# Optimization experiments

Hardware: AMD Instinct MI355X
Metric: run time of the kernel (lower is better)

## Reference

```python
import jax, jax.numpy as jnp
import numpy as np

D_K = 64

def setup_inputs() -> dict:
    key = jax.random.key(0)
    kq, kk, kv, km = jax.random.split(key, 4)
    B, H, S, D = 2, 16, 2048, D_K
    Q = jax.random.normal(kq, (B, H, S, D), dtype=jnp.float32)
    K = jax.random.normal(kk, (B, H, S, D), dtype=jnp.float32)
    V = jax.random.normal(kv, (B, H, S, D), dtype=jnp.float32)
    attn_mask = jax.random.bernoulli(km, 0.9, (B, H, S))  # True = valid
    return {"Q": Q, "K": K, "V": V, "attn_mask": attn_mask}

def reference(Q, K, V, attn_mask):
    # scores: [B, H, S, S]
    scores = jnp.einsum('bhqd,bhkd->bhqk', Q, K) / np.sqrt(D_K).astype(np.float32)
    fill = jnp.float32(1e-9)
    # mask rows (query positions) then columns (key positions), as in original
    scores = jnp.where(attn_mask[..., :, None], scores, fill)
    scores = jnp.where(attn_mask[..., None, :], scores, fill)
    attn = jax.nn.softmax(scores, axis=-1)
    context = jnp.einsum('bhqk,bhkd->bhqd', attn, V)
    return (context, attn)
```

## Files before the change

### kernel.cpp

```cpp
#include <hip/hip_runtime.h>

#define B_DIM 2
#define H_DIM 16
#define S_DIM 2048
#define D_DIM 64

constexpr int QB = 128;
constexpr int KB = 64;
constexpr int NT = S_DIM / KB;
constexpr float CL2E = 0.18033688011112042f;

typedef __attribute__((ext_vector_type(8))) short short8;
typedef __attribute__((ext_vector_type(4))) float f32x4;
typedef __attribute__((ext_vector_type(2))) unsigned uint2v;

__device__ __forceinline__ unsigned pkbf(float lo, float hi) {
  unsigned r;
  asm("v_cvt_pk_bf16_f32 %0, %1, %2" : "=v"(r) : "v"(lo), "v"(hi));
  return r;
}

__device__ __forceinline__ float fexp2(float x) {
  float r;
  asm("v_exp_f32 %0, %1" : "=v"(r) : "v"(x));
  return r;
}

__device__ __forceinline__ void barrier_lds() {
  asm volatile("s_waitcnt lgkmcnt(0)" ::: "memory");
  __builtin_amdgcn_s_barrier();
  asm volatile("" ::: "memory");
}

__global__ __launch_bounds__(256, 2)
void sdpa_kernel(const float* __restrict__ Qp, const float* __restrict__ Kp,
                 const float* __restrict__ Vp, const int* __restrict__ maskp,
                 float* __restrict__ ctx, float* __restrict__ attn)
{
  __shared__ __align__(16) unsigned short sK[2][KB * 64];
  __shared__ __align__(16) unsigned short sV[2][64 * KB];
  __shared__ __align__(16) unsigned short sP[2][4][32 * 64];

  const int tid  = threadIdx.x;
  const int wave = tid >> 6;
  const int lane = tid & 63;
  const int c = lane & 15;
  const int g = lane >> 4;

  const int bid = (blockIdx.x & 7) * 64 + (blockIdx.x >> 3);
  const int bh = bid >> 4;
  const int qt = bid & 15;
  const int q0 = qt * QB + wave * 32;
  const size_t bhS = (size_t)bh * S_DIM;

  const int key = tid >> 2;
  const int dq  = (tid & 3) << 4;
  const int kp  = (tid & 31) << 1;
  const int dq8 = (tid >> 5) << 3;

  short8 qf[2][2];
  #pragma unroll
  for (int m = 0; m < 2; ++m)
    #pragma unroll
    for (int kk = 0; kk < 2; ++kk) {
      const float* src = Qp + (bhS + (size_t)(q0 + m*16 + c)) * D_DIM + kk*32 + g*8;
      float4 a = ((const float4*)src)[0];
      float4 b = ((const float4*)src)[1];
      union { unsigned u[4]; short8 s; } w;
      w.u[0] = pkbf(a.x, a.y); w.u[1] = pkbf(a.z, a.w);
      w.u[2] = pkbf(b.x, b.y); w.u[3] = pkbf(b.z, b.w);
      qf[m][kk] = w.s;
    }

  float rvS[2];
  #pragma unroll
  for (int m = 0; m < 2; ++m)
    rvS[m] = maskp[bhS + q0 + m*16 + c] ? CL2E : 0.0f;

  float4 kr0, kr1, kr2, kr3;
  float4 vA0, vA1, vB0, vB1;
  unsigned kmr;

  auto load_k = [&](int kt_) {
    const float* s = Kp + (bhS + (size_t)(kt_ * KB + key)) * D_DIM + dq;
    kr0 = ((const float4*)s)[0]; kr1 = ((const float4*)s)[1];
    kr2 = ((const float4*)s)[2]; kr3 = ((const float4*)s)[3];
    kmr = maskp[bhS + kt_ * KB + key] ? 0xFFFFFFFFu : 0u;
  };
  auto load_v = [&](int kt_) {
    const float* s0 = Vp + (bhS + (size_t)(kt_ * KB + kp)) * D_DIM + dq8;
    vA0 = ((const float4*)s0)[0]; vA1 = ((const float4*)s0)[1];
    vB0 = ((const float4*)(s0 + D_DIM))[0]; vB1 = ((const float4*)(s0 + D_DIM))[1];
  };
  auto write_k = [&](int buf) {
    union { unsigned u[4]; short8 s; } w0, w1;
    w0.u[0] = pkbf(kr0.x, kr0.y) & kmr; w0.u[1] = pkbf(kr0.z, kr0.w) & kmr;
    w0.u[2] = pkbf(kr1.x, kr1.y) & kmr; w0.u[3] = pkbf(kr1.z, kr1.w) & kmr;
    w1.u[0] = pkbf(kr2.x, kr2.y) & kmr; w1.u[1] = pkbf(kr2.z, kr2.w) & kmr;
    w1.u[2] = pkbf(kr3.x, kr3.y) & kmr; w1.u[3] = pkbf(kr3.z, kr3.w) & kmr;
    const int sw = (key & 7) << 3;
    *(short8*)&sK[buf][key * 64 + (dq ^ sw)]       = w0.s;
    *(short8*)&sK[buf][key * 64 + ((dq + 8) ^ sw)] = w1.s;
  };
  auto write_v = [&](int buf) {
    float fa[8], fb[8];
    *(float4*)&fa[0] = vA0; *(float4*)&fa[4] = vA1;
    *(float4*)&fb[0] = vB0; *(float4*)&fb[4] = vB1;
    #pragma unroll
    for (int e = 0; e < 8; ++e) {
      const int d = dq8 + e;
      *(unsigned*)&sV[buf][d * KB + (kp ^ ((d & 7) << 3))] = pkbf(fa[e], fb[e]);
    }
  };

  float lsum[2] = {0.0f, 0.0f};

  load_k(0);
  for (int kt = 0; kt < NT; ++kt) {
    const int cur = kt & 1;
    write_k(cur);
    if (kt + 1 < NT) load_k(kt + 1);
    barrier_lds();

    short8 kf[4][2];
    #pragma unroll
    for (int n = 0; n < 4; ++n) {
      const int k2 = n*16 + c;
      const int sw = (c & 7) << 3;
      #pragma unroll
      for (int kk = 0; kk < 2; ++kk)
        kf[n][kk] = *(const short8*)&sK[cur][k2*64 + ((kk*32 + g*8) ^ sw)];
    }

    f32x4 sacc[4][2];
    #pragma unroll
    for (int n = 0; n < 4; ++n)
      #pragma unroll
      for (int m = 0; m < 2; ++m) sacc[n][m] = 0.0f;
    __builtin_amdgcn_s_setprio(1);
    #pragma unroll
    for (int n = 0; n < 4; ++n)
      #pragma unroll
      for (int m = 0; m < 2; ++m)
        #pragma unroll
        for (int kk = 0; kk < 2; ++kk)
          sacc[n][m] = __builtin_amdgcn_mfma_f32_16x16x32_bf16(kf[n][kk], qf[m][kk], sacc[n][m], 0, 0, 0);
    __builtin_amdgcn_s_setprio(0);

    #pragma unroll
    for (int m = 0; m < 2; ++m)
      #pragma unroll
      for (int n = 0; n < 4; ++n)
        #pragma unroll
        for (int e = 0; e < 4; ++e)
          lsum[m] += fexp2(sacc[n][m][e] * rvS[m]);
  }

  float Lm[2];
  #pragma unroll
  for (int m = 0; m < 2; ++m) {
    float v = lsum[m];
    v += __shfl_xor(v, 16);
    v += __shfl_xor(v, 32);
    Lm[m] = -__log2f(v);
  }

  f32x4 oacc[2][4];
  #pragma unroll
  for (int m = 0; m < 2; ++m)
    #pragma unroll
    for (int n = 0; n < 4; ++n) oacc[m][n] = 0.0f;

  const int rh  = lane >> 4;
  const int c16 = lane & 15;
  float* const abase = attn + (bhS + (size_t)q0) * S_DIM;

  auto copyout = [&](int pb, int kt_) {
    const unsigned short* const Pp = sP[pb][wave];
    float* const at = abase + kt_*KB;
    #pragma unroll
    for (int j = 0; j < 8; ++j) {
      const int rr = j*4 + rh;
      const int p8 = (c16 >> 1) ^ (rr & 7);
      uint2v u = *(const uint2v*)&Pp[rr*64 + p8*8 + (c16 & 1)*4];
      union { unsigned iu; float f; } t0, t1, t2, t3;
      t0.iu = u.x << 16; t1.iu = u.x & 0xFFFF0000u;
      t2.iu = u.y << 16; t3.iu = u.y & 0xFFFF0000u;
      f32x4 o; o[0] = t0.f; o[1] = t1.f; o[2] = t2.f; o[3] = t3.f;
      __builtin_nontemporal_store(o, (f32x4*)(at + (size_t)rr * S_DIM + c16*4));
    }
  };

  load_k(0); load_v(0);
  for (int kt = 0; kt < NT; ++kt) {
    const int cur = kt & 1;
    write_k(cur);
    write_v(cur);
    if (kt + 1 < NT) { load_k(kt + 1); load_v(kt + 1); }
    barrier_lds();

    short8 kf[4][2];
    #pragma unroll
    for (int n = 0; n < 4; ++n) {
      const int k2 = n*16 + c;
      const int sw = (c & 7) << 3;
      #pragma unroll
      for (int kk = 0; kk < 2; ++kk)
        kf[n][kk] = *(const short8*)&sK[cur][k2*64 + ((kk*32 + g*8) ^ sw)];
    }

    f32x4 sacc[4][2];
    #pragma unroll
    for (int n = 0; n < 4; ++n)
      #pragma unroll
      for (int m = 0; m < 2; ++m) sacc[n][m] = 0.0f;
    __builtin_amdgcn_s_setprio(1);
    #pragma unroll
    for (int n = 0; n < 4; ++n)
      #pragma unroll
      for (int m = 0; m < 2; ++m)
        #pragma unroll
        for (int kk = 0; kk < 2; ++kk)
          sacc[n][m] = __builtin_amdgcn_mfma_f32_16x16x32_bf16(kf[n][kk], qf[m][kk], sacc[n][m], 0, 0, 0);
    __builtin_amdgcn_s_setprio(0);

    if (kt > 0) copyout(cur ^ 1, kt - 1);

    unsigned short* const myP = sP[cur][wave];
    #pragma unroll
    for (int m = 0; m < 2; ++m) {
      #pragma unroll
      for (int n = 0; n < 4; ++n) {
        f32x4 pv;
        #pragma unroll
        for (int e = 0; e < 4; ++e)
          pv[e] = fexp2(__builtin_fmaf(sacc[n][m][e], rvS[m], Lm[m]));
        const int row = m*16 + c;
        const int swk = (n*16 + g*4) ^ ((c & 7) << 3);
        uint2v pr; pr.x = pkbf(pv[0], pv[1]); pr.y = pkbf(pv[2], pv[3]);
        *(uint2v*)&myP[row*64 + swk] = pr;
      }
    }

    short8 pf[2][2];
    #pragma unroll
    for (int m = 0; m < 2; ++m) {
      const int row = m*16 + c;
      const int sw = (c & 7) << 3;
      #pragma unroll
      for (int kk = 0; kk < 2; ++kk)
        pf[m][kk] = *(const short8*)&myP[row*64 + ((kk*32 + g*8) ^ sw)];
    }
    short8 vf[4][2];
    #pragma unroll
    for (int n = 0; n < 4; ++n) {
      const int d = n*16 + c;
      const int sw = (d & 7) << 3;
      #pragma unroll
      for (int kk = 0; kk < 2; ++kk)
        vf[n][kk] = *(const short8*)&sV[cur][d*KB + ((kk*32 + g*8) ^ sw)];
    }
    __builtin_amdgcn_s_setprio(1);
    #pragma unroll
    for (int m = 0; m < 2; ++m)
      #pragma unroll
      for (int n = 0; n < 4; ++n)
        #pragma unroll
        for (int kk = 0; kk < 2; ++kk)
          oacc[m][n] = __builtin_amdgcn_mfma_f32_16x16x32_bf16(pf[m][kk], vf[n][kk], oacc[m][n], 0, 0, 0);
    __builtin_amdgcn_s_setprio(0);
  }

  copyout((NT - 1) & 1, NT - 1);

  #pragma unroll
  for (int m = 0; m < 2; ++m)
    #pragma unroll
    for (int n = 0; n < 4; ++n)
      #pragma unroll
      for (int e = 0; e < 4; ++e) {
        const int rl = m*16 + g*4 + e;
        ctx[(bhS + (size_t)(q0 + rl)) * D_DIM + (size_t)(n*16 + c)] = oacc[m][n][e];
      }
}

extern "C" void kernel_launch(void* const* d_in, const int* in_sizes, int n_in,
                              void* d_out, int out_size, void* d_ws, size_t ws_size,
                              hipStream_t stream) {
  const float* Q = (const float*)d_in[0];
  const float* K = (const float*)d_in[1];
  const float* V = (const float*)d_in[2];
  const int*   M = (const int*)d_in[3];
  float* ctx  = (float*)d_out;
  float* attn = ctx + (size_t)B_DIM * H_DIM * S_DIM * D_DIM;
  dim3 grid(B_DIM * H_DIM * (S_DIM / QB));
  sdpa_kernel<<<grid, 256, 0, stream>>>(Q, K, V, M, ctx, attn);
}
```

Baseline: 152.9 us.

## Halve query tile to 16 rows per wave and raise occupancy to 4 blocks

The query block shrinks from 128 to 64 rows, so each wave handles 16 query rows instead of 32. The grid doubles and launch bounds request 4 blocks per CU. The P staging buffer loses its double buffer, and the attention copy-out now runs in the same iteration instead of lagging one tile. This aims to lower register and LDS pressure and raise occupancy to hide latency on the memory-bound attention-matrix write, but each K/V tile is now loaded and converted by twice as many blocks, and the copy-out no longer overlaps the next tile's MFMA work.

```diff
diff --git a/kernel.cpp b/kernel.cpp
--- a/kernel.cpp
+++ b/kernel.cpp
@@ -5,7 +5,7 @@
 #define S_DIM 2048
 #define D_DIM 64
 
-constexpr int QB = 128;
+constexpr int QB = 64;
 constexpr int KB = 64;
 constexpr int NT = S_DIM / KB;
 constexpr float CL2E = 0.18033688011112042f;
@@ -32,14 +32,14 @@
   asm volatile("" ::: "memory");
 }
 
-__global__ __launch_bounds__(256, 2)
+__global__ __launch_bounds__(256, 4)
 void sdpa_kernel(const float* __restrict__ Qp, const float* __restrict__ Kp,
                  const float* __restrict__ Vp, const int* __restrict__ maskp,
                  float* __restrict__ ctx, float* __restrict__ attn)
 {
   __shared__ __align__(16) unsigned short sK[2][KB * 64];
   __shared__ __align__(16) unsigned short sV[2][64 * KB];
-  __shared__ __align__(16) unsigned short sP[2][4][32 * 64];
+  __shared__ __align__(16) unsigned short sP[4][16 * 64];
 
   const int tid  = threadIdx.x;
   const int wave = tid >> 6;
@@ -47,10 +47,10 @@
   const int c = lane & 15;
   const int g = lane >> 4;
 
-  const int bid = (blockIdx.x & 7) * 64 + (blockIdx.x >> 3);
-  const int bh = bid >> 4;
-  const int qt = bid & 15;
-  const int q0 = qt * QB + wave * 32;
+  const int bid = (blockIdx.x & 7) * 128 + (blockIdx.x >> 3);
+  const int bh = bid >> 5;
+  const int qt = bid & 31;
+  const int q0 = qt * QB + wave * 16;
   const size_t bhS = (size_t)bh * S_DIM;
 
   const int key = tid >> 2;
@@ -58,24 +58,19 @@
   const int kp  = (tid & 31) << 1;
   const int dq8 = (tid >> 5) << 3;
 
-  short8 qf[2][2];
+  short8 qf[2];
   #pragma unroll
-  for (int m = 0; m < 2; ++m)
-    #pragma unroll
-    for (int kk = 0; kk < 2; ++kk) {
-      const float* src = Qp + (bhS + (size_t)(q0 + m*16 + c)) * D_DIM + kk*32 + g*8;
-      float4 a = ((const float4*)src)[0];
-      float4 b = ((const float4*)src)[1];
-      union { unsigned u[4]; short8 s; } w;
-      w.u[0] = pkbf(a.x, a.y); w.u[1] = pkbf(a.z, a.w);
-      w.u[2] = pkbf(b.x, b.y); w.u[3] = pkbf(b.z, b.w);
-      qf[m][kk] = w.s;
-    }
-
-  float rvS[2];
-  #pragma unroll
-  for (int m = 0; m < 2; ++m)
-    rvS[m] = maskp[bhS + q0 + m*16 + c] ? CL2E : 0.0f;
+  for (int kk = 0; kk < 2; ++kk) {
+    const float* src = Qp + (bhS + (size_t)(q0 + c)) * D_DIM + kk*32 + g*8;
+    float4 a = ((const float4*)src)[0];
+    float4 b = ((const float4*)src)[1];
+    union { unsigned u[4]; short8 s; } w;
+    w.u[0] = pkbf(a.x, a.y); w.u[1] = pkbf(a.z, a.w);
+    w.u[2] = pkbf(b.x, b.y); w.u[3] = pkbf(b.z, b.w);
+    qf[kk] = w.s;
+  }
+
+  const float rvS = maskp[bhS + q0 + c] ? CL2E : 0.0f;
 
   float4 kr0, kr1, kr2, kr3;
   float4 vA0, vA1, vB0, vB1;
@@ -113,7 +108,7 @@
     }
   };
 
-  float lsum[2] = {0.0f, 0.0f};
+  float lsum = 0.0f;
 
   load_k(0);
   for (int kt = 0; kt < NT; ++kt) {
@@ -132,57 +127,48 @@
         kf[n][kk] = *(const short8*)&sK[cur][k2*64 + ((kk*32 + g*8) ^ sw)];
     }
 
-    f32x4 sacc[4][2];
+    f32x4 sacc[4];
+    #pragma unroll
+    for (int n = 0; n < 4; ++n) sacc[n] = 0.0f;
+    __builtin_amdgcn_s_setprio(1);
     #pragma unroll
     for (int n = 0; n < 4; ++n)
       #pragma unroll
-      for (int m = 0; m < 2; ++m) sacc[n][m] = 0.0f;
-    __builtin_amdgcn_s_setprio(1);
+      for (int kk = 0; kk < 2; ++kk)
+        sacc[n] = __builtin_amdgcn_mfma_f32_16x16x32_bf16(kf[n][kk], qf[kk], sacc[n], 0, 0, 0);
+    __builtin_amdgcn_s_setprio(0);
+
     #pragma unroll
     for (int n = 0; n < 4; ++n)
       #pragma unroll
-      for (int m = 0; m < 2; ++m)
-        #pragma unroll
-        for (int kk = 0; kk < 2; ++kk)
-          sacc[n][m] = __builtin_amdgcn_mfma_f32_16x16x32_bf16(kf[n][kk], qf[m][kk], sacc[n][m], 0, 0, 0);
-    __builtin_amdgcn_s_setprio(0);
-
-    #pragma unroll
-    for (int m = 0; m < 2; ++m)
-      #pragma unroll
-      for (int n = 0; n < 4; ++n)
-        #pragma unroll
-        for (int e = 0; e < 4; ++e)
-          lsum[m] += fexp2(sacc[n][m][e] * rvS[m]);
-  }
-
-  float Lm[2];
-  #pragma unroll
-  for (int m = 0; m < 2; ++m) {
-    float v = lsum[m];
+      for (int e = 0; e < 4; ++e)
+        lsum += fexp2(sacc[n][e] * rvS);
+  }
+
+  float Lm;
+  {
+    float v = lsum;
     v += __shfl_xor(v, 16);
     v += __shfl_xor(v, 32);
-    Lm[m] = -__log2f(v);
-  }
-
-  f32x4 oacc[2][4];
+    Lm = -__log2f(v);
+  }
+
+  f32x4 oacc[4];
   #pragma unroll
-  for (int m = 0; m < 2; ++m)
-    #pragma unroll
-    for (int n = 0; n < 4; ++n) oacc[m][n] = 0.0f;
-
+  for (int n = 0; n < 4; ++n) oacc[n] = 0.0f;
+
+  unsigned short* const myP = sP[wave];
   const int rh  = lane >> 4;
   const int c16 = lane & 15;
   float* const abase = attn + (bhS + (size_t)q0) * S_DIM;
 
-  auto copyout = [&](int pb, int kt_) {
-    const unsigned short* const Pp = sP[pb][wave];
+  auto copyout = [&](int kt_) {
     float* const at = abase + kt_*KB;
     #pragma unroll
-    for (int j = 0; j < 8; ++j) {
+    for (int j = 0; j < 4; ++j) {
       const int rr = j*4 + rh;
       const int p8 = (c16 >> 1) ^ (rr & 7);
-      uint2v u = *(const uint2v*)&Pp[rr*64 + p8*8 + (c16 & 1)*4];
+      uint2v u = *(const uint2v*)&myP[rr*64 + p8*8 + (c16 & 1)*4];
       union { unsigned iu; float f; } t0, t1, t2, t3;
       t0.iu = u.x << 16; t1.iu = u.x & 0xFFFF0000u;
       t2.iu = u.y << 16; t3.iu = u.y & 0xFFFF0000u;
@@ -209,79 +195,55 @@
         kf[n][kk] = *(const short8*)&sK[cur][k2*64 + ((kk*32 + g*8) ^ sw)];
     }
 
-    f32x4 sacc[4][2];
+    f32x4 sacc[4];
+    #pragma unroll
+    for (int n = 0; n < 4; ++n) sacc[n] = 0.0f;
+    __builtin_amdgcn_s_setprio(1);
     #pragma unroll
     for (int n = 0; n < 4; ++n)
       #pragma unroll
-      for (int m = 0; m < 2; ++m) sacc[n][m] = 0.0f;
+      for (int kk = 0; kk < 2; ++kk)
+        sacc[n] = __builtin_amdgcn_mfma_f32_16x16x32_bf16(kf[n][kk], qf[kk], sacc[n], 0, 0, 0);
+    __builtin_amdgcn_s_setprio(0);
+
+    #pragma unroll
+    for (int n = 0; n < 4; ++n) {
+      f32x4 pv;
+      #pragma unroll
+      for (int e = 0; e < 4; ++e)
+        pv[e] = fexp2(__builtin_fmaf(sacc[n][e], rvS, Lm));
+      const int swk = (n*16 + g*4) ^ ((c & 7) << 3);
+      uint2v pr; pr.x = pkbf(pv[0], pv[1]); pr.y = pkbf(pv[2], pv[3]);
+      *(uint2v*)&myP[c*64 + swk] = pr;
+    }
+
+    short8 pf[2];
+    #pragma unroll
+    for (int kk = 0; kk < 2; ++kk)
+      pf[kk] = *(const short8*)&myP[c*64 + ((kk*32 + g*8) ^ ((c & 7) << 3))];
     __builtin_amdgcn_s_setprio(1);
-    #pragma unroll
-    for (int n = 0; n < 4; ++n)
-      #pragma unroll
-      for (int m = 0; m < 2; ++m)
-        #pragma unroll
-        for (int kk = 0; kk < 2; ++kk)
-          sacc[n][m] = __builtin_amdgcn_mfma_f32_16x16x32_bf16(kf[n][kk], qf[m][kk], sacc[n][m], 0, 0, 0);
-    __builtin_amdgcn_s_setprio(0);
-
-    if (kt > 0) copyout(cur ^ 1, kt - 1);
-
-    unsigned short* const myP = sP[cur][wave];
-    #pragma unroll
-    for (int m = 0; m < 2; ++m) {
-      #pragma unroll
-      for (int n = 0; n < 4; ++n) {
-        f32x4 pv;
-        #pragma unroll
-        for (int e = 0; e < 4; ++e)
-          pv[e] = fexp2(__builtin_fmaf(sacc[n][m][e], rvS[m], Lm[m]));
-        const int row = m*16 + c;
-        const int swk = (n*16 + g*4) ^ ((c & 7) << 3);
-        uint2v pr; pr.x = pkbf(pv[0], pv[1]); pr.y = pkbf(pv[2], pv[3]);
-        *(uint2v*)&myP[row*64 + swk] = pr;
-      }
-    }
-
-    short8 pf[2][2];
-    #pragma unroll
-    for (int m = 0; m < 2; ++m) {
-      const int row = m*16 + c;
-      const int sw = (c & 7) << 3;
-      #pragma unroll
-      for (int kk = 0; kk < 2; ++kk)
-        pf[m][kk] = *(const short8*)&myP[row*64 + ((kk*32 + g*8) ^ sw)];
-    }
-    short8 vf[4][2];
     #pragma unroll
     for (int n = 0; n < 4; ++n) {
       const int d = n*16 + c;
       const int sw = (d & 7) << 3;
       #pragma unroll
-      for (int kk = 0; kk < 2; ++kk)
-        vf[n][kk] = *(const short8*)&sV[cur][d*KB + ((kk*32 + g*8) ^ sw)];
-    }
-    __builtin_amdgcn_s_setprio(1);
-    #pragma unroll
-    for (int m = 0; m < 2; ++m)
-      #pragma unroll
-      for (int n = 0; n < 4; ++n)
-        #pragma unroll
-        for (int kk = 0; kk < 2; ++kk)
-          oacc[m][n] = __builtin_amdgcn_mfma_f32_16x16x32_bf16(pf[m][kk], vf[n][kk], oacc[m][n], 0, 0, 0);
+      for (int kk = 0; kk < 2; ++kk) {
+        short8 vf = *(const short8*)&sV[cur][d*KB + ((kk*32 + g*8) ^ sw)];
+        oacc[n] = __builtin_amdgcn_mfma_f32_16x16x32_bf16(pf[kk], vf, oacc[n], 0, 0, 0);
+      }
+    }
     __builtin_amdgcn_s_setprio(0);
-  }
-
-  copyout((NT - 1) & 1, NT - 1);
+
+    copyout(kt);
+  }
 
   #pragma unroll
-  for (int m = 0; m < 2; ++m)
-    #pragma unroll
-    for (int n = 0; n < 4; ++n)
-      #pragma unroll
-      for (int e = 0; e < 4; ++e) {
-        const int rl = m*16 + g*4 + e;
-        ctx[(bhS + (size_t)(q0 + rl)) * D_DIM + (size_t)(n*16 + c)] = oacc[m][n][e];
-      }
+  for (int n = 0; n < 4; ++n)
+    #pragma unroll
+    for (int e = 0; e < 4; ++e) {
+      const int rl = g*4 + e;
+      ctx[(bhS + (size_t)(q0 + rl)) * D_DIM + (size_t)(n*16 + c)] = oacc[n][e];
+    }
 }
 
 extern "C" void kernel_launch(void* const* d_in, const int* in_sizes, int n_in,
```

New measurement: 161.7 us. 1.06x slower.

## Split softmax row-sum pass into a separate higher-occupancy kernel

Applied to the files above, without the earlier changes.

Moves the first pass, which computes the log-sum-exp per query row, out of the main attention kernel into its own kernel. That kernel uses smaller query tiles (64 rows per block, 16 per wave), needs only K in LDS, and is allowed 4 blocks per CU. It writes the row normalisers to workspace, and the main kernel reads them back before doing the second pass that writes attn and ctx. This adds a launch and a small workspace round trip, and the second kernel still recomputes QK^T in exchange for better occupancy in the first pass.

```diff
diff --git a/kernel.cpp b/kernel.cpp
--- a/kernel.cpp
+++ b/kernel.cpp
@@ -5,7 +5,6 @@
 #define S_DIM 2048
 #define D_DIM 64
 
-constexpr int QB = 128;
 constexpr int KB = 64;
 constexpr int NT = S_DIM / KB;
 constexpr float CL2E = 0.18033688011112042f;
@@ -32,14 +31,11 @@
   asm volatile("" ::: "memory");
 }
 
-__global__ __launch_bounds__(256, 2)
-void sdpa_kernel(const float* __restrict__ Qp, const float* __restrict__ Kp,
-                 const float* __restrict__ Vp, const int* __restrict__ maskp,
-                 float* __restrict__ ctx, float* __restrict__ attn)
+__global__ __launch_bounds__(256, 4)
+void rowsum_kernel(const float* __restrict__ Qp, const float* __restrict__ Kp,
+                   const int* __restrict__ maskp, float* __restrict__ LmOut)
 {
   __shared__ __align__(16) unsigned short sK[2][KB * 64];
-  __shared__ __align__(16) unsigned short sV[2][64 * KB];
-  __shared__ __align__(16) unsigned short sP[2][4][32 * 64];
 
   const int tid  = threadIdx.x;
   const int wave = tid >> 6;
@@ -47,50 +43,36 @@
   const int c = lane & 15;
   const int g = lane >> 4;
 
-  const int bid = (blockIdx.x & 7) * 64 + (blockIdx.x >> 3);
-  const int bh = bid >> 4;
-  const int qt = bid & 15;
-  const int q0 = qt * QB + wave * 32;
+  const int bid = (blockIdx.x & 7) * 128 + (blockIdx.x >> 3);
+  const int bh = bid >> 5;
+  const int qt = bid & 31;
+  const int q0 = qt * 64 + wave * 16;
   const size_t bhS = (size_t)bh * S_DIM;
 
   const int key = tid >> 2;
   const int dq  = (tid & 3) << 4;
-  const int kp  = (tid & 31) << 1;
-  const int dq8 = (tid >> 5) << 3;
-
-  short8 qf[2][2];
-  #pragma unroll
-  for (int m = 0; m < 2; ++m)
-    #pragma unroll
-    for (int kk = 0; kk < 2; ++kk) {
-      const float* src = Qp + (bhS + (size_t)(q0 + m*16 + c)) * D_DIM + kk*32 + g*8;
-      float4 a = ((const float4*)src)[0];
-      float4 b = ((const float4*)src)[1];
-      union { unsigned u[4]; short8 s; } w;
-      w.u[0] = pkbf(a.x, a.y); w.u[1] = pkbf(a.z, a.w);
-      w.u[2] = pkbf(b.x, b.y); w.u[3] = pkbf(b.z, b.w);
-      qf[m][kk] = w.s;
-    }
-
-  float rvS[2];
-  #pragma unroll
-  for (int m = 0; m < 2; ++m)
-    rvS[m] = maskp[bhS + q0 + m*16 + c] ? CL2E : 0.0f;
+
+  short8 qf[2];
+  #pragma unroll
+  for (int kk = 0; kk < 2; ++kk) {
+    const float* src = Qp + (bhS + (size_t)(q0 + c)) * D_DIM + kk*32 + g*8;
+    float4 a = ((const float4*)src)[0];
+    float4 b = ((const float4*)src)[1];
+    union { unsigned u[4]; short8 s; } w;
+    w.u[0] = pkbf(a.x, a.y); w.u[1] = pkbf(a.z, a.w);
+    w.u[2] = pkbf(b.x, b.y); w.u[3] = pkbf(b.z, b.w);
+    qf[kk] = w.s;
+  }
+
+  const float rvS = maskp[bhS + q0 + c] ? CL2E : 0.0f;
 
   float4 kr0, kr1, kr2, kr3;
-  float4 vA0, vA1, vB0, vB1;
   unsigned kmr;
-
   auto load_k = [&](int kt_) {
     const float* s = Kp + (bhS + (size_t)(kt_ * KB + key)) * D_DIM + dq;
     kr0 = ((const float4*)s)[0]; kr1 = ((const float4*)s)[1];
     kr2 = ((const float4*)s)[2]; kr3 = ((const float4*)s)[3];
     kmr = maskp[bhS + kt_ * KB + key] ? 0xFFFFFFFFu : 0u;
-  };
-  auto load_v = [&](int kt_) {
-    const float* s0 = Vp + (bhS + (size_t)(kt_ * KB + kp)) * D_DIM + dq8;
-    vA0 = ((const float4*)s0)[0]; vA1 = ((const float4*)s0)[1];
-    vB0 = ((const float4*)(s0 + D_DIM))[0]; vB1 = ((const float4*)(s0 + D_DIM))[1];
   };
   auto write_k = [&](int buf) {
     union { unsigned u[4]; short8 s; } w0, w1;
@@ -102,19 +84,8 @@
     *(short8*)&sK[buf][key * 64 + (dq ^ sw)]       = w0.s;
     *(short8*)&sK[buf][key * 64 + ((dq + 8) ^ sw)] = w1.s;
   };
-  auto write_v = [&](int buf) {
-    float fa[8], fb[8];
-    *(float4*)&fa[0] = vA0; *(float4*)&fa[4] = vA1;
-    *(float4*)&fb[0] = vB0; *(float4*)&fb[4] = vB1;
-    #pragma unroll
-    for (int e = 0; e < 8; ++e) {
-      const int d = dq8 + e;
-      *(unsigned*)&sV[buf][d * KB + (kp ^ ((d & 7) << 3))] = pkbf(fa[e], fb[e]);
-    }
-  };
-
-  float lsum[2] = {0.0f, 0.0f};
-
+
+  float lsum = 0.0f;
   load_k(0);
   for (int kt = 0; kt < NT; ++kt) {
     const int cur = kt & 1;
@@ -132,38 +103,113 @@
         kf[n][kk] = *(const short8*)&sK[cur][k2*64 + ((kk*32 + g*8) ^ sw)];
     }
 
-    f32x4 sacc[4][2];
-    #pragma unroll
-    for (int n = 0; n < 4; ++n)
-      #pragma unroll
-      for (int m = 0; m < 2; ++m) sacc[n][m] = 0.0f;
+    f32x4 sacc[4];
+    #pragma unroll
+    for (int n = 0; n < 4; ++n) sacc[n] = 0.0f;
     __builtin_amdgcn_s_setprio(1);
     #pragma unroll
     for (int n = 0; n < 4; ++n)
       #pragma unroll
-      for (int m = 0; m < 2; ++m)
-        #pragma unroll
-        for (int kk = 0; kk < 2; ++kk)
-          sacc[n][m] = __builtin_amdgcn_mfma_f32_16x16x32_bf16(kf[n][kk], qf[m][kk], sacc[n][m], 0, 0, 0);
+      for (int kk = 0; kk < 2; ++kk)
+        sacc[n] = __builtin_amdgcn_mfma_f32_16x16x32_bf16(kf[n][kk], qf[kk], sacc[n], 0, 0, 0);
     __builtin_amdgcn_s_setprio(0);
 
     #pragma unroll
-    for (int m = 0; m < 2; ++m)
-      #pragma unroll
-      for (int n = 0; n < 4; ++n)
-        #pragma unroll
-        for (int e = 0; e < 4; ++e)
-          lsum[m] += fexp2(sacc[n][m][e] * rvS[m]);
+    for (int n = 0; n < 4; ++n)
+      #pragma unroll
+      for (int e = 0; e < 4; ++e)
+        lsum += fexp2(sacc[n][e] * rvS);
   }
 
-  float Lm[2];
+  float v = lsum;
+  v += __shfl_xor(v, 16);
+  v += __shfl_xor(v, 32);
+  if (g == 0) LmOut[bhS + q0 + c] = -__log2f(v);
+}
+
+__global__ __launch_bounds__(256, 2)
+void sdpa_kernel(const float* __restrict__ Qp, const float* __restrict__ Kp,
+                 const float* __restrict__ Vp, const int* __restrict__ maskp,
+                 const float* __restrict__ LmIn,
+                 float* __restrict__ ctx, float* __restrict__ attn)
+{
+  __shared__ __align__(16) unsigned short sK[2][KB * 64];
+  __shared__ __align__(16) unsigned short sV[2][64 * KB];
+  __shared__ __align__(16) unsigned short sP[2][4][32 * 64];
+
+  const int tid  = threadIdx.x;
+  const int wave = tid >> 6;
+  const int lane = tid & 63;
+  const int c = lane & 15;
+  const int g = lane >> 4;
+
+  const int bid = (blockIdx.x & 7) * 64 + (blockIdx.x >> 3);
+  const int bh = bid >> 4;
+  const int qt = bid & 15;
+  const int q0 = qt * 128 + wave * 32;
+  const size_t bhS = (size_t)bh * S_DIM;
+
+  const int key = tid >> 2;
+  const int dq  = (tid & 3) << 4;
+  const int kp  = (tid & 31) << 1;
+  const int dq8 = (tid >> 5) << 3;
+
+  short8 qf[2][2];
+  #pragma unroll
+  for (int m = 0; m < 2; ++m)
+    #pragma unroll
+    for (int kk = 0; kk < 2; ++kk) {
+      const float* src = Qp + (bhS + (size_t)(q0 + m*16 + c)) * D_DIM + kk*32 + g*8;
+      float4 a = ((const float4*)src)[0];
+      float4 b = ((const float4*)src)[1];
+      union { unsigned u[4]; short8 s; } w;
+      w.u[0] = pkbf(a.x, a.y); w.u[1] = pkbf(a.z, a.w);
+      w.u[2] = pkbf(b.x, b.y); w.u[3] = pkbf(b.z, b.w);
+      qf[m][kk] = w.s;
+    }
+
+  float rvS[2], Lm[2];
   #pragma unroll
   for (int m = 0; m < 2; ++m) {
-    float v = lsum[m];
-    v += __shfl_xor(v, 16);
-    v += __shfl_xor(v, 32);
-    Lm[m] = -__log2f(v);
+    rvS[m] = maskp[bhS + q0 + m*16 + c] ? CL2E : 0.0f;
+    Lm[m]  = LmIn[bhS + q0 + m*16 + c];
   }
+
+  float4 kr0, kr1, kr2, kr3;
+  float4 vA0, vA1, vB0, vB1;
+  unsigned kmr;
+
+  auto load_k = [&](int kt_) {
+    const float* s = Kp + (bhS + (size_t)(kt_ * KB + key)) * D_DIM + dq;
+    kr0 = ((const float4*)s)[0]; kr1 = ((const float4*)s)[1];
+    kr2 = ((const float4*)s)[2]; kr3 = ((const float4*)s)[3];
+    kmr = maskp[bhS + kt_ * KB + key] ? 0xFFFFFFFFu : 0u;
+  };
+  auto load_v = [&](int kt_) {
+    const float* s0 = Vp + (bhS + (size_t)(kt_ * KB + kp)) * D_DIM + dq8;
+    vA0 = ((const float4*)s0)[0]; vA1 = ((const float4*)s0)[1];
+    vB0 = ((const float4*)(s0 + D_DIM))[0]; vB1 = ((const float4*)(s0 + D_DIM))[1];
+  };
+  auto write_k = [&](int buf) {
+    union { unsigned u[4]; short8 s; } w0, w1;
+    w0.u[0] = pkbf(kr0.x, kr0.y) & kmr; w0.u[1] = pkbf(kr0.z, kr0.w) & kmr;
+    w0.u[2] = pkbf(kr1.x, kr1.y) & kmr; w0.u[3] = pkbf(kr1.z, kr1.w) & kmr;
+    w1.u[0] = pkbf(kr2.x, kr2.y) & kmr; w1.u[1] = pkbf(kr2.z, kr2.w) & kmr;
+    w1.u[2] = pkbf(kr3.x, kr3.y) & kmr; w1.u[3] = pkbf(kr3.z, kr3.w) & kmr;
+    const int sw = (key & 7) << 3;
+    *(short8*)&sK[buf][key * 64 + (dq ^ sw)]       = w0.s;
+    *(short8*)&sK[buf][key * 64 + ((dq + 8) ^ sw)] = w1.s;
+  };
+  auto write_v = [&](int buf) {
+    float fa[8], fb[8];
+    *(float4*)&fa[0] = vA0; *(float4*)&fa[4] = vA1;
+    *(float4*)&fb[0] = vB0; *(float4*)&fb[4] = vB1;
+    #pragma unroll
+    for (int e = 0; e < 8; ++e) {
+      const int d = dq8 + e;
+      *(unsigned*)&sV[buf][d * KB + (kp ^ ((d & 7) << 3))] = pkbf(fa[e], fb[e]);
+    }
+  };
 
   f32x4 oacc[2][4];
   #pragma unroll
@@ -293,6 +339,8 @@
   const int*   M = (const int*)d_in[3];
   float* ctx  = (float*)d_out;
   float* attn = ctx + (size_t)B_DIM * H_DIM * S_DIM * D_DIM;
-  dim3 grid(B_DIM * H_DIM * (S_DIM / QB));
-  sdpa_kernel<<<grid, 256, 0, stream>>>(Q, K, V, M, ctx, attn);
-}
+  float* Lms  = (float*)d_ws;
+
+  rowsum_kernel<<<dim3(B_DIM * H_DIM * (S_DIM / 64)), 256, 0, stream>>>(Q, K, M, Lms);
+  sdpa_kernel<<<dim3(B_DIM * H_DIM * (S_DIM / 128)), 256, 0, stream>>>(Q, K, V, M, Lms, ctx, attn);
+}
```

New measurement: 170.5 us. +11.5%, slower.
